# Kernel optimization log

Hardware: AMD Instinct MI355X
Metric: run time of the kernel (lower is better)

Reference implementation:

```python
import jax, jax.numpy as jnp
import numpy as np

NUM_GRAPHS = 4096


def setup_inputs() -> dict:
    key = jax.random.key(0)
    k1, k2, k3, k4 = jax.random.split(key, 4)
    N, H = 500000, 256
    x = jax.random.normal(k1, (N, H), dtype=jnp.float32)
    batch = jnp.sort(jax.random.randint(k2, (N,), 0, NUM_GRAPHS, dtype=jnp.int64))
    W1 = jax.random.normal(k3, (H, H), dtype=jnp.float32) * (1.0 / np.sqrt(H))
    b1 = jnp.zeros((H,), dtype=jnp.float32)
    w2 = jax.random.normal(k4, (H, 1), dtype=jnp.float32) * (1.0 / np.sqrt(H))
    return {"x": x, "batch": batch, "W1": W1, "b1": b1, "w2": w2}


def reference(x, batch, W1, b1, w2):
    # attention scores: Linear -> Tanh -> Linear(no bias)  -> [N, 1]
    scores = jnp.tanh(x @ W1 + b1) @ w2  # [N, 1]
    # Torch code scatter-maxes into a zeros buffer, so the effective per-graph
    # max is clamped below at 0 (faithfully replicated here).
    seg_max = jax.ops.segment_max(scores, batch, num_segments=NUM_GRAPHS)  # [G, 1]
    seg_max = jnp.maximum(seg_max, 0.0)
    exp_scores = jnp.exp(scores - seg_max[batch])  # [N, 1]
    sum_exp = jax.ops.segment_sum(exp_scores, batch, num_segments=NUM_GRAPHS)  # [G, 1]
    normalized = exp_scores / sum_exp[batch]  # [N, 1]
    graph_embedding = jax.ops.segment_sum(x * normalized, batch, num_segments=NUM_GRAPHS)  # [G, H]
    return graph_embedding
```

## Files before the change

### kernel.cpp

```cpp
#include <hip/hip_runtime.h>
#include <hip/hip_bf16.h>
#include <cstdint>

#define H 256
#define BK 32
#define MT 64
#define ROWS 128

typedef _Float16 half8 __attribute__((ext_vector_type(8)));
typedef float floatx4 __attribute__((ext_vector_type(4)));

__device__ __forceinline__ float fast_tanh(float v) {
    v = fminf(fmaxf(v, -15.f), 15.f);
    float e = __expf(2.f * v);
    return (e - 1.f) / (e + 1.f);
}

__global__ void init_kernel(float* __restrict__ out, int* __restrict__ maxv,
                            float* __restrict__ sumexp, int G, int total) {
    int i = blockIdx.x * 256 + threadIdx.x;
    if (i < total) out[i] = 0.f;
    if (i < G) { maxv[i] = 0; sumexp[i] = 0.f; }
}

__global__ void w1conv_kernel(const float* __restrict__ W1, _Float16* __restrict__ w1c) {
    int i = blockIdx.x * 256 + threadIdx.x;
    if (i < H * H) {
        int j = i >> 8, k = i & 255;
        w1c[i] = (_Float16)W1[k * H + j];
    }
}

__global__ __launch_bounds__(256) void scores_kernel(
    const float* __restrict__ x, const _Float16* __restrict__ w1c,
    const float* __restrict__ b1, const float* __restrict__ w2,
    float* __restrict__ scores, int N) {
    __shared__ _Float16 As[MT][BK];
    __shared__ float sred[4][MT];

    const int tid = threadIdx.x;
    const int wv = tid >> 6;
    const int lane = tid & 63;
    const int m = lane & 15;
    const int q = lane >> 4;
    const int row0 = blockIdx.x * MT;

    floatx4 acc[4][4] = {};

    const int r_st = tid >> 2;
    const int g_st = tid & 3;
    const int gs = g_st ^ ((r_st >> 1) & 3);
    const int rg = q ^ ((m >> 1) & 3);

    for (int kk = 0; kk < H; kk += BK) {
        float4 f0, f1;
        int grow = row0 + r_st;
        if (grow < N) {
            const float* src = x + (size_t)grow * H + kk + g_st * 8;
            f0 = *(const float4*)src;
            f1 = *(const float4*)(src + 4);
        } else {
            f0 = make_float4(0.f, 0.f, 0.f, 0.f);
            f1 = f0;
        }
        half8 hv;
        hv[0] = (_Float16)f0.x; hv[1] = (_Float16)f0.y;
        hv[2] = (_Float16)f0.z; hv[3] = (_Float16)f0.w;
        hv[4] = (_Float16)f1.x; hv[5] = (_Float16)f1.y;
        hv[6] = (_Float16)f1.z; hv[7] = (_Float16)f1.w;
        __syncthreads();
        *(half8*)&As[r_st][gs * 8] = hv;
        __syncthreads();

        half8 af[4];
#pragma unroll
        for (int mi = 0; mi < 4; ++mi)
            af[mi] = *(const half8*)&As[mi * 16 + m][rg * 8];
        half8 bf[4];
#pragma unroll
        for (int ni = 0; ni < 4; ++ni) {
            int c = wv * 64 + ni * 16 + m;
            bf[ni] = *(const half8*)(w1c + (size_t)c * H + kk + q * 8);
        }
#pragma unroll
        for (int mi = 0; mi < 4; ++mi)
#pragma unroll
            for (int ni = 0; ni < 4; ++ni)
                acc[mi][ni] = __builtin_amdgcn_mfma_f32_16x16x32_f16(
                    af[mi], bf[ni], acc[mi][ni], 0, 0, 0);
    }

    float b1c[4], w2c[4];
#pragma unroll
    for (int ni = 0; ni < 4; ++ni) {
        int c = wv * 64 + ni * 16 + m;
        b1c[ni] = b1[c];
        w2c[ni] = w2[c];
    }
#pragma unroll
    for (int mi = 0; mi < 4; ++mi) {
#pragma unroll
        for (int r = 0; r < 4; ++r) {
            float v = 0.f;
#pragma unroll
            for (int ni = 0; ni < 4; ++ni)
                v += w2c[ni] * fast_tanh(acc[mi][ni][r] + b1c[ni]);
            v += __shfl_xor(v, 1);
            v += __shfl_xor(v, 2);
            v += __shfl_xor(v, 4);
            v += __shfl_xor(v, 8);
            if (m == 0) sred[wv][mi * 16 + q * 4 + r] = v;
        }
    }
    __syncthreads();
    if (tid < MT) {
        int row = row0 + tid;
        if (row < N)
            scores[row] = sred[0][tid] + sred[1][tid] + sred[2][tid] + sred[3][tid];
    }
}

__global__ void segmax_kernel(const float* __restrict__ scores,
                              const int* __restrict__ batch,
                              int* __restrict__ maxv, int N) {
    int i = blockIdx.x * 256 + threadIdx.x;
    if (i < N) {
        float s = scores[i];
        if (s > 0.f) atomicMax(&maxv[batch[i]], __float_as_int(s));
    }
}

__global__ __launch_bounds__(256) void pass2_kernel(
    const float* __restrict__ x, const int* __restrict__ batch,
    const float* __restrict__ scores, const int* __restrict__ maxv,
    float* __restrict__ out, float* __restrict__ sumexp, int N) {
    const int t = threadIdx.x;
    int i0 = blockIdx.x * ROWS;
    if (i0 >= N) return;
    int i1 = min(i0 + ROWS, N);

    float acc = 0.f, sw = 0.f;
    int cur = batch[i0];

    float xv = x[(size_t)i0 * H + t];
    int g = cur;
    float w = __expf(scores[i0] - __int_as_float(maxv[g]));

    for (int i = i0; i < i1; ++i) {
        float xv_n = 0.f, w_n = 0.f;
        int g_n = cur;
        if (i + 1 < i1) {
            xv_n = x[(size_t)(i + 1) * H + t];
            g_n = batch[i + 1];
            w_n = __expf(scores[i + 1] - __int_as_float(maxv[g_n]));
        }
        if (g != cur) {
            atomicAdd(&out[(size_t)cur * H + t], acc);
            if (t == 0) atomicAdd(&sumexp[cur], sw);
            acc = 0.f;
            sw = 0.f;
            cur = g;
        }
        acc = fmaf(w, xv, acc);
        if (t == 0) sw += w;
        xv = xv_n; g = g_n; w = w_n;
    }
    atomicAdd(&out[(size_t)cur * H + t], acc);
    if (t == 0) atomicAdd(&sumexp[cur], sw);
}

__global__ void normalize_kernel(float* __restrict__ out,
                                 const float* __restrict__ sumexp, int total) {
    int i = blockIdx.x * 256 + threadIdx.x;
    if (i < total) {
        float s = sumexp[i >> 8];
        out[i] = (s > 0.f) ? out[i] / s : 0.f;
    }
}

extern "C" void kernel_launch(void* const* d_in, const int* in_sizes, int n_in,
                              void* d_out, int out_size, void* d_ws, size_t ws_size,
                              hipStream_t stream) {
    const float* x = (const float*)d_in[0];
    const int* batch = (const int*)d_in[1];
    const float* W1 = (const float*)d_in[2];
    const float* b1 = (const float*)d_in[3];
    const float* w2 = (const float*)d_in[4];
    float* out = (float*)d_out;

    const int N = in_sizes[0] / H;
    const int G = out_size / H;

    char* ws = (char*)d_ws;
    float* scores = (float*)ws;
    size_t off = (size_t)N * sizeof(float);
    off = (off + 15) & ~(size_t)15;
    int* maxv = (int*)(ws + off);
    off += (size_t)G * sizeof(int);
    float* sumexp = (float*)(ws + off);
    off += (size_t)G * sizeof(float);
    off = (off + 15) & ~(size_t)15;
    _Float16* w1c = (_Float16*)(ws + off);

    int total = G * H;
    init_kernel<<<(total + 255) / 256, 256, 0, stream>>>(out, maxv, sumexp, G, total);
    w1conv_kernel<<<(H * H + 255) / 256, 256, 0, stream>>>(W1, w1c);
    scores_kernel<<<(N + MT - 1) / MT, 256, 0, stream>>>(x, w1c, b1, w2, scores, N);
    segmax_kernel<<<(N + 255) / 256, 256, 0, stream>>>(scores, batch, maxv, N);
    pass2_kernel<<<(N + ROWS - 1) / ROWS, 256, 0, stream>>>(x, batch, scores, maxv, out, sumexp, N);
    normalize_kernel<<<(total + 255) / 256, 256, 0, stream>>>(out, sumexp, total);
}
```

Baseline: 968.0 us.

## Double-buffer scores GEMM, fuse segment max, and vectorize pooling pass

```diff
diff --git a/kernel.cpp b/kernel.cpp
--- a/kernel.cpp
+++ b/kernel.cpp
@@ -1,11 +1,9 @@
 #include <hip/hip_runtime.h>
-#include <hip/hip_bf16.h>
 #include <cstdint>
 
 #define H 256
-#define BK 32
 #define MT 64
-#define ROWS 128
+#define ROWS 256
 
 typedef _Float16 half8 __attribute__((ext_vector_type(8)));
 typedef float floatx4 __attribute__((ext_vector_type(4)));
@@ -16,27 +14,34 @@
     return (e - 1.f) / (e + 1.f);
 }
 
-__global__ void init_kernel(float* __restrict__ out, int* __restrict__ maxv,
-                            float* __restrict__ sumexp, int G, int total) {
+__global__ void init_kernel(float4* __restrict__ out4, int* __restrict__ maxv,
+                            float* __restrict__ sumexp, int G, int total4) {
     int i = blockIdx.x * 256 + threadIdx.x;
-    if (i < total) out[i] = 0.f;
+    if (i < total4) out4[i] = make_float4(0.f, 0.f, 0.f, 0.f);
     if (i < G) { maxv[i] = 0; sumexp[i] = 0.f; }
 }
 
 __global__ void w1conv_kernel(const float* __restrict__ W1, _Float16* __restrict__ w1c) {
     int i = blockIdx.x * 256 + threadIdx.x;
     if (i < H * H) {
-        int j = i >> 8, k = i & 255;
-        w1c[i] = (_Float16)W1[k * H + j];
-    }
-}
-
-__global__ __launch_bounds__(256) void scores_kernel(
+        int r = i & 511;
+        int lane = r >> 3, h = r & 7;
+        int t = i >> 9;
+        int kc = t & 1, s = (t >> 1) & 3, ct = t >> 3;
+        int mm = lane & 15, qq = lane >> 4;
+        int col = ct * 16 + mm;
+        int k = s * 64 + kc * 32 + qq * 8 + h;
+        w1c[i] = (_Float16)W1[k * H + col];
+    }
+}
+
+__global__ __launch_bounds__(256, 3) void scores_kernel(
     const float* __restrict__ x, const _Float16* __restrict__ w1c,
     const float* __restrict__ b1, const float* __restrict__ w2,
-    float* __restrict__ scores, int N) {
-    __shared__ _Float16 As[MT][BK];
-    __shared__ float sred[4][MT];
+    const int* __restrict__ batch,
+    float* __restrict__ scores, int* __restrict__ maxv, int N) {
+    __shared__ _Float16 As[2][64][64];
+    __shared__ float sred[4][64];
 
     const int tid = threadIdx.x;
     const int wv = tid >> 6;
@@ -45,49 +50,77 @@
     const int q = lane >> 4;
     const int row0 = blockIdx.x * MT;
 
+    const int srow = tid >> 2;
+    const int sc4 = tid & 3;
+    const int sg0 = (sc4 * 2) ^ (srow & 7);
+    const int sg1 = (sc4 * 2 + 1) ^ (srow & 7);
+    const bool srok = (row0 + srow) < N;
+    const float* sbase = x + (size_t)(row0 + srow) * H + sc4 * 16;
+
     floatx4 acc[4][4] = {};
 
-    const int r_st = tid >> 2;
-    const int g_st = tid & 3;
-    const int gs = g_st ^ ((r_st >> 1) & 3);
-    const int rg = q ^ ((m >> 1) & 3);
-
-    for (int kk = 0; kk < H; kk += BK) {
-        float4 f0, f1;
-        int grow = row0 + r_st;
-        if (grow < N) {
-            const float* src = x + (size_t)grow * H + kk + g_st * 8;
-            f0 = *(const float4*)src;
-            f1 = *(const float4*)(src + 4);
-        } else {
-            f0 = make_float4(0.f, 0.f, 0.f, 0.f);
-            f1 = f0;
-        }
-        half8 hv;
-        hv[0] = (_Float16)f0.x; hv[1] = (_Float16)f0.y;
-        hv[2] = (_Float16)f0.z; hv[3] = (_Float16)f0.w;
-        hv[4] = (_Float16)f1.x; hv[5] = (_Float16)f1.y;
-        hv[6] = (_Float16)f1.z; hv[7] = (_Float16)f1.w;
+    float4 f0, f1, f2, f3;
+    f0 = f1 = f2 = f3 = make_float4(0.f, 0.f, 0.f, 0.f);
+    if (srok) {
+        const float4* p = (const float4*)sbase;
+        f0 = p[0]; f1 = p[1]; f2 = p[2]; f3 = p[3];
+    }
+    {
+        half8 h0, h1;
+        h0[0] = (_Float16)f0.x; h0[1] = (_Float16)f0.y; h0[2] = (_Float16)f0.z; h0[3] = (_Float16)f0.w;
+        h0[4] = (_Float16)f1.x; h0[5] = (_Float16)f1.y; h0[6] = (_Float16)f1.z; h0[7] = (_Float16)f1.w;
+        h1[0] = (_Float16)f2.x; h1[1] = (_Float16)f2.y; h1[2] = (_Float16)f2.z; h1[3] = (_Float16)f2.w;
+        h1[4] = (_Float16)f3.x; h1[5] = (_Float16)f3.y; h1[6] = (_Float16)f3.z; h1[7] = (_Float16)f3.w;
+        *(half8*)&As[0][srow][sg0 * 8] = h0;
+        *(half8*)&As[0][srow][sg1 * 8] = h1;
+    }
+    __syncthreads();
+
+    for (int s = 0; s < 4; ++s) {
+        const int cur = s & 1;
+        if (s < 3 && srok) {
+            const float4* p = (const float4*)(sbase + (s + 1) * 64);
+            f0 = p[0]; f1 = p[1]; f2 = p[2]; f3 = p[3];
+        }
+        half8 bf[4][2];
+#pragma unroll
+        for (int ni = 0; ni < 4; ++ni) {
+            int ct = wv * 4 + ni;
+#pragma unroll
+            for (int kc = 0; kc < 2; ++kc) {
+                int chunk = ((ct << 2) | s) * 2 + kc;
+                bf[ni][kc] = *(const half8*)(w1c + ((size_t)chunk << 9) + lane * 8);
+            }
+        }
+        half8 af[4][2];
+#pragma unroll
+        for (int mi = 0; mi < 4; ++mi) {
+            int r = mi * 16 + m;
+#pragma unroll
+            for (int kc = 0; kc < 2; ++kc) {
+                int g = (kc * 4 + q) ^ (r & 7);
+                af[mi][kc] = *(const half8*)&As[cur][r][g * 8];
+            }
+        }
+#pragma unroll
+        for (int mi = 0; mi < 4; ++mi)
+#pragma unroll
+            for (int ni = 0; ni < 4; ++ni) {
+                acc[mi][ni] = __builtin_amdgcn_mfma_f32_16x16x32_f16(
+                    af[mi][0], bf[ni][0], acc[mi][ni], 0, 0, 0);
+                acc[mi][ni] = __builtin_amdgcn_mfma_f32_16x16x32_f16(
+                    af[mi][1], bf[ni][1], acc[mi][ni], 0, 0, 0);
+            }
+        if (s < 3) {
+            half8 h0, h1;
+            h0[0] = (_Float16)f0.x; h0[1] = (_Float16)f0.y; h0[2] = (_Float16)f0.z; h0[3] = (_Float16)f0.w;
+            h0[4] = (_Float16)f1.x; h0[5] = (_Float16)f1.y; h0[6] = (_Float16)f1.z; h0[7] = (_Float16)f1.w;
+            h1[0] = (_Float16)f2.x; h1[1] = (_Float16)f2.y; h1[2] = (_Float16)f2.z; h1[3] = (_Float16)f2.w;
+            h1[4] = (_Float16)f3.x; h1[5] = (_Float16)f3.y; h1[6] = (_Float16)f3.z; h1[7] = (_Float16)f3.w;
+            *(half8*)&As[1 - cur][srow][sg0 * 8] = h0;
+            *(half8*)&As[1 - cur][srow][sg1 * 8] = h1;
+        }
         __syncthreads();
-        *(half8*)&As[r_st][gs * 8] = hv;
-        __syncthreads();
-
-        half8 af[4];
-#pragma unroll
-        for (int mi = 0; mi < 4; ++mi)
-            af[mi] = *(const half8*)&As[mi * 16 + m][rg * 8];
-        half8 bf[4];
-#pragma unroll
-        for (int ni = 0; ni < 4; ++ni) {
-            int c = wv * 64 + ni * 16 + m;
-            bf[ni] = *(const half8*)(w1c + (size_t)c * H + kk + q * 8);
-        }
-#pragma unroll
-        for (int mi = 0; mi < 4; ++mi)
-#pragma unroll
-            for (int ni = 0; ni < 4; ++ni)
-                acc[mi][ni] = __builtin_amdgcn_mfma_f32_16x16x32_f16(
-                    af[mi], bf[ni], acc[mi][ni], 0, 0, 0);
     }
 
     float b1c[4], w2c[4];
@@ -115,18 +148,11 @@
     __syncthreads();
     if (tid < MT) {
         int row = row0 + tid;
-        if (row < N)
-            scores[row] = sred[0][tid] + sred[1][tid] + sred[2][tid] + sred[3][tid];
-    }
-}
-
-__global__ void segmax_kernel(const float* __restrict__ scores,
-                              const int* __restrict__ batch,
-                              int* __restrict__ maxv, int N) {
-    int i = blockIdx.x * 256 + threadIdx.x;
-    if (i < N) {
-        float s = scores[i];
-        if (s > 0.f) atomicMax(&maxv[batch[i]], __float_as_int(s));
+        if (row < N) {
+            float sc = sred[0][tid] + sred[1][tid] + sred[2][tid] + sred[3][tid];
+            scores[row] = sc;
+            if (sc > 0.f) atomicMax(&maxv[batch[row]], __float_as_int(sc));
+        }
     }
 }
 
@@ -135,46 +161,66 @@
     const float* __restrict__ scores, const int* __restrict__ maxv,
     float* __restrict__ out, float* __restrict__ sumexp, int N) {
     const int t = threadIdx.x;
-    int i0 = blockIdx.x * ROWS;
-    if (i0 >= N) return;
-    int i1 = min(i0 + ROWS, N);
-
-    float acc = 0.f, sw = 0.f;
-    int cur = batch[i0];
-
-    float xv = x[(size_t)i0 * H + t];
+    const int sub = t >> 6;
+    const int lane = t & 63;
+    const int base = blockIdx.x * ROWS;
+    const int i1 = min(base + ROWS, N);
+    int i = base + sub;
+    if (i >= i1) return;
+
+    const float4* x4 = (const float4*)x;
+
+    float ax = 0.f, ay = 0.f, az = 0.f, aw = 0.f, sw = 0.f;
+    int cur = batch[i];
     int g = cur;
-    float w = __expf(scores[i0] - __int_as_float(maxv[g]));
-
-    for (int i = i0; i < i1; ++i) {
-        float xv_n = 0.f, w_n = 0.f;
-        int g_n = cur;
-        if (i + 1 < i1) {
-            xv_n = x[(size_t)(i + 1) * H + t];
-            g_n = batch[i + 1];
-            w_n = __expf(scores[i + 1] - __int_as_float(maxv[g_n]));
+    float4 xv = x4[(size_t)i * 64 + lane];
+    float w = __expf(scores[i] - __int_as_float(maxv[cur]));
+
+    while (i < i1) {
+        int inx = i + 4;
+        float4 xv_n = make_float4(0.f, 0.f, 0.f, 0.f);
+        float w_n = 0.f;
+        int g_n = g;
+        if (inx < i1) {
+            xv_n = x4[(size_t)inx * 64 + lane];
+            g_n = batch[inx];
+            w_n = __expf(scores[inx] - __int_as_float(maxv[g_n]));
         }
         if (g != cur) {
-            atomicAdd(&out[(size_t)cur * H + t], acc);
-            if (t == 0) atomicAdd(&sumexp[cur], sw);
-            acc = 0.f;
-            sw = 0.f;
+            float* o = out + (size_t)cur * H + lane * 4;
+            atomicAdd(o + 0, ax); atomicAdd(o + 1, ay);
+            atomicAdd(o + 2, az); atomicAdd(o + 3, aw);
+            if (lane == 0) atomicAdd(&sumexp[cur], sw);
+            ax = ay = az = aw = 0.f; sw = 0.f;
             cur = g;
         }
-        acc = fmaf(w, xv, acc);
-        if (t == 0) sw += w;
-        xv = xv_n; g = g_n; w = w_n;
-    }
-    atomicAdd(&out[(size_t)cur * H + t], acc);
-    if (t == 0) atomicAdd(&sumexp[cur], sw);
-}
-
-__global__ void normalize_kernel(float* __restrict__ out,
-                                 const float* __restrict__ sumexp, int total) {
+        ax = fmaf(w, xv.x, ax);
+        ay = fmaf(w, xv.y, ay);
+        az = fmaf(w, xv.z, az);
+        aw = fmaf(w, xv.w, aw);
+        if (lane == 0) sw += w;
+        xv = xv_n; w = w_n; g = g_n;
+        i = inx;
+    }
+    float* o = out + (size_t)cur * H + lane * 4;
+    atomicAdd(o + 0, ax); atomicAdd(o + 1, ay);
+    atomicAdd(o + 2, az); atomicAdd(o + 3, aw);
+    if (lane == 0) atomicAdd(&sumexp[cur], sw);
+}
+
+__global__ void normalize_kernel(float4* __restrict__ out4,
+                                 const float* __restrict__ sumexp, int total4) {
     int i = blockIdx.x * 256 + threadIdx.x;
-    if (i < total) {
-        float s = sumexp[i >> 8];
-        out[i] = (s > 0.f) ? out[i] / s : 0.f;
+    if (i < total4) {
+        float s = sumexp[i >> 6];
+        if (s > 0.f) {
+            float inv = 1.f / s;
+            float4 v = out4[i];
+            v.x *= inv; v.y *= inv; v.z *= inv; v.w *= inv;
+            out4[i] = v;
+        } else {
+            out4[i] = make_float4(0.f, 0.f, 0.f, 0.f);
+        }
     }
 }
 
@@ -202,11 +248,14 @@
     off = (off + 15) & ~(size_t)15;
     _Float16* w1c = (_Float16*)(ws + off);
 
-    int total = G * H;
-    init_kernel<<<(total + 255) / 256, 256, 0, stream>>>(out, maxv, sumexp, G, total);
+    const int total4 = (G * H) / 4;
+    init_kernel<<<(max(total4, G) + 255) / 256, 256, 0, stream>>>(
+        (float4*)out, maxv, sumexp, G, total4);
     w1conv_kernel<<<(H * H + 255) / 256, 256, 0, stream>>>(W1, w1c);
-    scores_kernel<<<(N + MT - 1) / MT, 256, 0, stream>>>(x, w1c, b1, w2, scores, N);
-    segmax_kernel<<<(N + 255) / 256, 256, 0, stream>>>(scores, batch, maxv, N);
-    pass2_kernel<<<(N + ROWS - 1) / ROWS, 256, 0, stream>>>(x, batch, scores, maxv, out, sumexp, N);
-    normalize_kernel<<<(total + 255) / 256, 256, 0, stream>>>(out, sumexp, total);
-}
+    scores_kernel<<<(N + MT - 1) / MT, 256, 0, stream>>>(
+        x, w1c, b1, w2, batch, scores, maxv, N);
+    pass2_kernel<<<(N + ROWS - 1) / ROWS, 256, 0, stream>>>(
+        x, batch, scores, maxv, out, sumexp, N);
+    normalize_kernel<<<(total4 + 255) / 256, 256, 0, stream>>>(
+        (float4*)out, sumexp, total4);
+}
```

Measured after the change: 912.4 us. -5.7%, faster.
